# Optimization experiments

Hardware: AMD Instinct MI355X
Metric: run time of the kernel (lower is better)

The kernel has to match this reference:

```python
import jax, jax.numpy as jnp
import numpy as np

IN_DIM = 768
OUT_DIM = 768


def setup_inputs() -> dict:
    key = jax.random.key(0)
    k_x, k_q, k_k, k_v = jax.random.split(key, 4)
    B, S = 4, 4096
    x = jax.random.normal(k_x, (B, S, IN_DIM), dtype=jnp.float32)
    scale = 1.0 / np.sqrt(IN_DIM)
    Wq = jax.random.normal(k_q, (IN_DIM, OUT_DIM), dtype=jnp.float32) * scale
    Wk = jax.random.normal(k_k, (IN_DIM, OUT_DIM), dtype=jnp.float32) * scale
    Wv = jax.random.normal(k_v, (IN_DIM, OUT_DIM), dtype=jnp.float32) * scale
    return {"x": x, "Wq": Wq, "Wk": Wk, "Wv": Wv}


def reference(x, Wq, Wk, Wv):
    # x: [B, S, D_in]; W*: [D_in, D_out] (Linear without bias)
    q = jnp.einsum('bsd,de->bse', x, Wq)
    k = jnp.einsum('bsd,de->bse', x, Wk)
    v = jnp.einsum('bsd,de->bse', x, Wv)
    S = x.shape[1]
    scores = jnp.einsum('bqe,bke->bqk', q, k)  # [B, S, S]
    causal = jnp.tril(jnp.ones((S, S), dtype=bool))  # True where allowed
    scores = jnp.where(causal[None], scores, -jnp.inf)
    scale = 1.0 / jnp.sqrt(jnp.asarray(q.shape[-1], dtype=scores.dtype))
    weights = jax.nn.softmax(scores * scale, axis=-1)
    # dropout p=0.0 -> identity
    return jnp.einsum('bqk,bke->bqe', weights, v)
```

## Files before the change

kernel.cpp:

```cpp
#include <hip/hip_runtime.h>
#include <hip/hip_bf16.h>
#include <hip/hip_fp16.h>

#define DIM 768
#define SLEN 4096
#define BATCH 4
#define NTILES 528
#define NT256 136
#define SPB ((size_t)NTILES * 16384)

typedef __attribute__((ext_vector_type(8))) short short8;
typedef __attribute__((ext_vector_type(4))) short short4v;
typedef __attribute__((ext_vector_type(4))) float f32x4;
typedef __attribute__((ext_vector_type(8))) _Float16 f16x8;

typedef __attribute__((address_space(1))) void gvoid;
typedef __attribute__((address_space(3))) void lvoid;

__device__ __forceinline__ void gl_lds16(const void* g, void* l) {
  __builtin_amdgcn_global_load_lds((gvoid*)g, (lvoid*)l, 16, 0, 0);
}

__device__ __forceinline__ unsigned short f2h(float x) {
  union { _Float16 h; unsigned short u; } c; c.h = (_Float16)x; return c.u;
}
__device__ __forceinline__ float h2f(unsigned short u) {
  union { _Float16 h; unsigned short u; } c; c.u = u; return (float)c.h;
}

union V8 { short8 v; unsigned short u[8]; };

__global__ __launch_bounds__(256) void convert_x_kernel(
    const float* __restrict__ x, unsigned short* __restrict__ xb) {
  size_t i = ((size_t)blockIdx.x * 256 + threadIdx.x) * 8;
  f32x4 a = *(const f32x4*)(x + i);
  f32x4 b = *(const f32x4*)(x + i + 4);
  V8 o;
#pragma unroll
  for (int j = 0; j < 4; ++j) { o.u[j] = f2h(a[j]); o.u[4 + j] = f2h(b[j]); }
  *(short8*)(xb + i) = o.v;
}

__global__ __launch_bounds__(256) void transpose_w_kernel(
    const float* __restrict__ Wq, const float* __restrict__ Wk,
    const float* __restrict__ Wv, unsigned short* __restrict__ Wt) {
  __shared__ float Tl[32][33];
  const float* Wi = blockIdx.z == 0 ? Wq : (blockIdx.z == 1 ? Wk : Wv);
  unsigned short* Wo = Wt + (size_t)blockIdx.z * DIM * DIM;
  int k0 = blockIdx.x * 32, n0 = blockIdx.y * 32;
  int t = threadIdx.x;
  int r = t >> 3, c4 = (t & 7) * 4;
  f32x4 v = *(const f32x4*)(Wi + (size_t)(k0 + r) * DIM + n0 + c4);
#pragma unroll
  for (int j = 0; j < 4; ++j) Tl[r][c4 + j] = v[j];
  __syncthreads();
  short4v ov;
#pragma unroll
  for (int j = 0; j < 4; ++j) ov[j] = (short)f2h(Tl[c4 + j][r]);
  *(short4v*)(Wo + (size_t)(n0 + r) * DIM + k0 + c4) = ov;
}


#define STAGE(src, row0, kb, ldsoff)                                              \
  {                                                                               \
    gl_lds16((src) + (size_t)((row0) + rA) * DIM + (kb) + cA,                     \
             ldsb + (ldsoff) + t * 16);                                           \
    gl_lds16((src) + (size_t)((row0) + 64 + rA) * DIM + (kb) + cA,                \
             ldsb + (ldsoff) + 8192 + t * 16);                                    \
  }

#define STAGEP(srcp, stride, ldsoff)                                              \
  {                                                                               \
    gl_lds16((srcp) + (size_t)rA * (stride) + cA, ldsb + (ldsoff) + t * 16);      \
    gl_lds16((srcp) + (size_t)(64 + rA) * (stride) + cA,                          \
             ldsb + (ldsoff) + 8192 + t * 16);                                    \
  }

#define QPHASE(MH, CHB, STG, VMW)                                                 \
  {                                                                               \
    f16x8 afr[4];                                                                 \
    _Pragma("unroll") for (int j = 0; j < 4; ++j)                                 \
        afr[j] = __builtin_bit_cast(f16x8, *(const short8*)(ldsb + aB +           \
                 (MH) * 16384 + (j * 32 + arow) * 128 + (CHB)));                  \
    if ((MH) == 0) {                                                              \
      _Pragma("unroll") for (int n = 0; n < 4; ++n)                               \
          bfr[n] = __builtin_bit_cast(f16x8, *(const short8*)(ldsb + bB +         \
                   bh * 16384 + (brow + n * 16) * 128 + (CHB)));                  \
    }                                                                             \
    STG;                                                                          \
    VMW;                                                                          \
    asm volatile("s_barrier" ::: "memory");                                       \
    asm volatile("s_waitcnt lgkmcnt(0)" ::: "memory");                            \
    __builtin_amdgcn_sched_barrier(0);                                            \
    __builtin_amdgcn_s_setprio(1);                                                \
    _Pragma("unroll") for (int j = 0; j < 4; ++j)                                 \
      _Pragma("unroll") for (int n = 0; n < 4; ++n)                               \
        acc[(MH) * 4 + j][n] = __builtin_amdgcn_mfma_f32_16x16x32_f16(            \
            afr[j], bfr[n], acc[(MH) * 4 + j][n], 0, 0, 0);                       \
    __builtin_amdgcn_s_setprio(0);                                                \
    __builtin_amdgcn_sched_barrier(0);                                            \
    asm volatile("s_barrier" ::: "memory");                                       \
  }

template <int MODE>
__global__ __launch_bounds__(512, 2) void gemm8_kernel(
    const unsigned short* __restrict__ Ag, const unsigned short* __restrict__ Bg,
    unsigned short* __restrict__ o0, unsigned short* __restrict__ o1,
    unsigned short* __restrict__ o2, size_t stAB, size_t stS) {
  __shared__ __align__(16) unsigned short lds[65536];
  char* ldsb = (char*)lds;
  const int t = threadIdx.x;
  const int lane = t & 63, w = t >> 6;
  const int l15 = lane & 15, lg = lane >> 4;
  const int wr = w >> 2, wc = w & 3;

  int m0, n0, qt = 0, kt = 0, z = 0;
  const unsigned short *A, *B;
  unsigned short* Co = nullptr;
  unsigned short* Sb = nullptr;
  if (MODE == 0) {
    const int o = blockIdx.x;
    const int oi = (o & 7) * 72 + (o >> 3);
    const int mt = oi / 9, sub = oi - mt * 9;
    const int ntile = sub / 3;
    z = sub - ntile * 3;
    if (z < 2) {
      m0 = mt * 256; n0 = ntile * 256;
      A = Ag; B = Bg + (size_t)z * DIM * DIM;
      Co = z == 0 ? o0 : o1;
    } else {
      m0 = ntile * 256; n0 = mt * 256;
      A = Bg + (size_t)2 * DIM * DIM; B = Ag;
      Co = o2;
    }
  } else {
    const int i0 = blockIdx.x, b = blockIdx.y;
    const int i = (i0 & 7) * 17 + (i0 >> 3);
    qt = (int)((sqrtf(8.f * i + 1.f) - 1.f) * 0.5f);
    while ((qt + 1) * (qt + 2) / 2 <= i) ++qt;
    while (qt * (qt + 1) / 2 > i) --qt;
    kt = i - qt * (qt + 1) / 2;
    m0 = qt * 256; n0 = kt * 256;
    A = Ag + (size_t)b * stAB; B = Bg + (size_t)b * stAB;
    Sb = o0 + (size_t)b * stS;
  }

  const int rA = t >> 3;
  const int cA = (((t & 7) ^ ((t >> 3) & 7)) << 3);
  const int ch0 = ((lg ^ (l15 & 7)) << 4);
  const int arow = wr * 16 + l15;
  const int bh = wc >> 1;
  const int brow = (wc & 1) * 64 + l15;

  f32x4 acc[8][4];
#pragma unroll
  for (int f = 0; f < 8; ++f)
#pragma unroll
    for (int n = 0; n < 4; ++n) acc[f][n] = f32x4{0.f, 0.f, 0.f, 0.f};

  STAGE(A, m0, 0, 0);
  STAGE(B, n0, 0, 65536);
  STAGE(B, n0 + 128, 0, 65536 + 16384);
  STAGE(A, m0 + 128, 0, 16384);
  STAGE(B, n0, 64, 65536 + 32768);
  STAGE(A, m0, 64, 32768);
  asm volatile("s_waitcnt vmcnt(4)" ::: "memory");
  asm volatile("s_barrier" ::: "memory");

  for (int tt = 0; tt < 12; ++tt) {
    const int bt = tt & 1;
    const int aB = bt * 32768;
    const int bB = 65536 + bt * 32768;
    const int aN = (1 - bt) * 32768;
    const int bN = 65536 + (1 - bt) * 32768;
    const int kb1 = (tt + 1 < 12 ? tt + 1 : 11) * 64;
    const int kb2 = (tt + 2 < 12 ? tt + 2 : 11) * 64;
    f16x8 bfr[4];
    QPHASE(0, ch0,
           STAGE(B, n0 + 128, kb1, bN + 16384); STAGE(A, m0 + 128, kb1, aN + 16384),
           (void)0);
    QPHASE(1, ch0, (void)0, (void)0);
    QPHASE(0, ch0 ^ 64, (void)0, (void)0);
    QPHASE(1, ch0 ^ 64,
           STAGE(B, n0, kb2, bB); STAGE(A, m0, kb2, aB),
           asm volatile("s_waitcnt vmcnt(4)" ::: "memory"));
  }
  asm volatile("s_waitcnt vmcnt(0)" ::: "memory");

  if (MODE == 0) {
    if (z < 2) {
#pragma unroll
      for (int f = 0; f < 8; ++f) {
        const int row = m0 + f * 32 + wr * 16 + lg * 4;
#pragma unroll
        for (int n = 0; n < 4; ++n) {
          const int col = n0 + wc * 64 + n * 16 + l15;
#pragma unroll
          for (int ii = 0; ii < 4; ++ii)
            Co[(size_t)(row + ii) * DIM + col] = f2h(acc[f][n][ii]);
        }
      }
    } else {
      const int bb = n0 >> 12;
      unsigned short* O = Co + (size_t)bb * DIM * SLEN;
#pragma unroll
      for (int f = 0; f < 8; ++f) {
        const int row = m0 + f * 32 + wr * 16 + lg * 4;
#pragma unroll
        for (int n = 0; n < 4; ++n) {
          const int sl = (n0 + wc * 64 + n * 16 + l15) & (SLEN - 1);
#pragma unroll
          for (int ii = 0; ii < 4; ++ii)
            O[(size_t)(row + ii) * SLEN + sl] = f2h(acc[f][n][ii]);
        }
      }
    }
  } else {
#pragma unroll
    for (int f = 0; f < 8; ++f) {
      const int rl = (f * 32 + wr * 16 + lg * 4) & 127;
      const int Q128 = qt * 2 + (f >= 4 ? 1 : 0);
      const int K128 = kt * 2 + (wc >> 1);
      if (K128 > Q128) continue;
      const size_t tb = (size_t)(Q128 * (Q128 + 1) / 2 + K128) * 16384;
#pragma unroll
      for (int n = 0; n < 4; ++n) {
        const int cl = ((wc & 1) * 64 + n * 16 + l15);
#pragma unroll
        for (int ii = 0; ii < 4; ++ii)
          Sb[tb + (size_t)(rl + ii) * 128 + cl] = f2h(acc[f][n][ii]);
      }
    }
  }
}

__global__ __launch_bounds__(256) void softmax_kernel(
    unsigned short* __restrict__ S, size_t s_bstride) {
  __shared__ float redm[4], reds[4];
  const int r = blockIdx.x, b = blockIdx.y;
  unsigned short* Sb = S + (size_t)b * s_bstride;
  const int qt = r >> 7, rl = r & 127;
  const int ncols = (qt + 1) * 128;
  const size_t rowbase = (size_t)(qt * (qt + 1) / 2) * 16384 + (size_t)rl * 128;
  const int t = threadIdx.x, lane = t & 63, w = t >> 6;
  const int c0 = t * 16;
  const bool act = c0 < ncols;
  const float NEG = -3.0e38f;
  float sv[16];
  unsigned short* p = nullptr;
  if (act) {
    int ktile = c0 >> 7, cl = c0 & 127;
    p = Sb + rowbase + (size_t)ktile * 16384 + cl;
    V8 v0, v1; v0.v = *(const short8*)p; v1.v = *(const short8*)(p + 8);
#pragma unroll
    for (int j = 0; j < 8; ++j) {
      sv[j] = (c0 + j > r) ? NEG : h2f(v0.u[j]);
      sv[8 + j] = (c0 + 8 + j > r) ? NEG : h2f(v1.u[j]);
    }
  } else {
#pragma unroll
    for (int j = 0; j < 16; ++j) sv[j] = NEG;
  }
  float mx = NEG;
#pragma unroll
  for (int j = 0; j < 16; ++j) mx = fmaxf(mx, sv[j]);
#pragma unroll
  for (int d = 1; d < 64; d <<= 1) mx = fmaxf(mx, __shfl_xor(mx, d));
  if (lane == 0) redm[w] = mx;
  __syncthreads();
  mx = fmaxf(fmaxf(redm[0], redm[1]), fmaxf(redm[2], redm[3]));
  const float scl = 1.4426950408889634f / 27.712812921102035f;
  float e[16], sm = 0.f;
#pragma unroll
  for (int j = 0; j < 16; ++j) { e[j] = exp2f((sv[j] - mx) * scl); sm += e[j]; }
#pragma unroll
  for (int d = 1; d < 64; d <<= 1) sm += __shfl_xor(sm, d);
  if (lane == 0) reds[w] = sm;
  __syncthreads();
  float inv = 1.0f / (reds[0] + reds[1] + reds[2] + reds[3]);
  if (act) {
    V8 o0, o1;
#pragma unroll
    for (int j = 0; j < 8; ++j) { o0.u[j] = f2h(e[j] * inv); o1.u[j] = f2h(e[8 + j] * inv); }
    *(short8*)p = o0.v;
    *(short8*)(p + 8) = o1.v;
  }
}

__global__ __launch_bounds__(256) void zero_tile_kernel(unsigned short* __restrict__ z) {
  ((short8*)z)[blockIdx.x * 256 + threadIdx.x] = short8{0, 0, 0, 0, 0, 0, 0, 0};
}

__device__ const int pv_mt[24]  = {15,15,7,14,14,13,13,6,12,12,11,11,5,10,10,9,9,4,8,8,3,2,1,0};
__device__ const int pv_ks0[24] = {0,32,0,0,30,0,28,0,0,26,0,24,0,0,22,0,20,0,0,18,0,0,0,0};
__device__ const int pv_kl[24]  = {32,32,32,30,30,28,28,28,26,26,24,24,24,22,22,20,20,20,18,18,16,12,8,4};
__device__ const int pv_sec[24] = {0,1,0,0,1,0,1,0,0,1,0,1,0,0,1,0,1,0,0,1,0,0,0,0};

__global__ __launch_bounds__(512, 2) void pv256_kernel(
    const unsigned short* __restrict__ S, const unsigned short* __restrict__ Vt,
    const unsigned short* __restrict__ Zt, float* __restrict__ Out,
    float* __restrict__ Part) {
  __shared__ __align__(16) unsigned short lds[65536];
  char* ldsb = (char*)lds;
  const int t = threadIdx.x, lane = t & 63, w = t >> 6;
  const int l15 = lane & 15, lg = lane >> 4;
  const int wr = w >> 2, wc = w & 3;
  const int rank = blockIdx.x / 12, sub = blockIdx.x % 12;
  const int b = sub / 3, nt = sub % 3;
  const int mt = pv_mt[rank], ks0 = pv_ks0[rank], kl = pv_kl[rank];
  const int sec = pv_sec[rank];
  const int q0 = 2 * mt, q1 = 2 * mt + 1;
  const int kend = ks0 + kl;
  const unsigned short* Sbb = S + (size_t)b * SPB;
  const unsigned short* Vb = Vt + (size_t)b * DIM * SLEN + (size_t)(nt * 256) * SLEN;

  auto asrc = [&](int ks, int qh) -> const unsigned short* {
    const int K128 = ks >> 1;
    const unsigned short* base =
        (K128 <= qh) ? Sbb + (size_t)(qh * (qh + 1) / 2 + K128) * 16384 : Zt;
    return base + (ks & 1) * 64;
  };

  const int rA = t >> 3;
  const int cA = (((t & 7) ^ ((t >> 3) & 7)) << 3);
  const int ch0 = ((lg ^ (l15 & 7)) << 4);
  const int arow = wr * 16 + l15;
  const int bh = wc >> 1;
  const int brow = (wc & 1) * 64 + l15;

  f32x4 acc[8][4];
#pragma unroll
  for (int f = 0; f < 8; ++f)
#pragma unroll
    for (int n = 0; n < 4; ++n) acc[f][n] = f32x4{0.f, 0.f, 0.f, 0.f};

  const int ksp = (ks0 + 1 < kend) ? ks0 + 1 : kend - 1;
  STAGEP(asrc(ks0, q0), 128, 0);
  STAGEP(Vb + (size_t)ks0 * 64, SLEN, 65536);
  STAGEP(Vb + (size_t)128 * SLEN + (size_t)ks0 * 64, SLEN, 65536 + 16384);
  STAGEP(asrc(ks0, q1), 128, 16384);
  STAGEP(Vb + (size_t)ksp * 64, SLEN, 65536 + 32768);
  STAGEP(asrc(ksp, q0), 128, 32768);
  asm volatile("s_waitcnt vmcnt(4)" ::: "memory");
  asm volatile("s_barrier" ::: "memory");

  for (int it = 0; it < kl; ++it) {
    const int ts = ks0 + it;
    const int bt = it & 1;
    const int aB = bt * 32768;
    const int bB = 65536 + bt * 32768;
    const int aN = (1 - bt) * 32768;
    const int bN = 65536 + (1 - bt) * 32768;
    const int t1 = (ts + 1 < kend) ? ts + 1 : kend - 1;
    const int t2 = (ts + 2 < kend) ? ts + 2 : kend - 1;
    f16x8 bfr[4];
    QPHASE(0, ch0,
           STAGEP(Vb + (size_t)128 * SLEN + (size_t)t1 * 64, SLEN, bN + 16384);
           STAGEP(asrc(t1, q1), 128, aN + 16384),
           (void)0);
    QPHASE(1, ch0, (void)0, (void)0);
    QPHASE(0, ch0 ^ 64, (void)0, (void)0);
    QPHASE(1, ch0 ^ 64,
           STAGEP(Vb + (size_t)t2 * 64, SLEN, bB);
           STAGEP(asrc(t2, q0), 128, aB),
           asm volatile("s_waitcnt vmcnt(4)" ::: "memory"));
  }
  asm volatile("s_waitcnt vmcnt(0)" ::: "memory");

  if (!sec) {
    float* Ob = Out + (size_t)b * SLEN * DIM + (size_t)(mt * 256) * DIM + nt * 256;
#pragma unroll
    for (int f = 0; f < 8; ++f) {
      const int rl = f * 32 + wr * 16 + lg * 4;
#pragma unroll
      for (int n = 0; n < 4; ++n) {
        const int cl = wc * 64 + n * 16 + l15;
#pragma unroll
        for (int ii = 0; ii < 4; ++ii)
          Ob[(size_t)(rl + ii) * DIM + cl] = acc[f][n][ii];
      }
    }
  } else {
    float* Pb = Part + (size_t)((b * 3 + nt) * 8 + (mt - 8)) * 65536;
#pragma unroll
    for (int f = 0; f < 8; ++f) {
      const int rl = f * 32 + wr * 16 + lg * 4;
#pragma unroll
      for (int n = 0; n < 4; ++n) {
        const int cl = wc * 64 + n * 16 + l15;
#pragma unroll
        for (int ii = 0; ii < 4; ++ii)
          Pb[(size_t)(rl + ii) * 256 + cl] = acc[f][n][ii];
      }
    }
  }
}

__global__ __launch_bounds__(256) void pv_reduce_kernel(
    const float* __restrict__ Part, float* __restrict__ Out) {
  const int bx = blockIdx.x;
  const int p = bx >> 6;
  const int within = ((bx & 63) * 256 + threadIdx.x) * 4;
  const int mt = 8 + (p & 7);
  const int bnt = p >> 3, b = bnt / 3, nt = bnt % 3;
  const int r = within >> 8, c = within & 255;
  float* o = Out + (size_t)b * SLEN * DIM + (size_t)(mt * 256 + r) * DIM + nt * 256 + c;
  const f32x4 pv = *(const f32x4*)(Part + (size_t)p * 65536 + within);
  const f32x4 ov = *(const f32x4*)o;
  *(f32x4*)o = ov + pv;
}

__global__ __launch_bounds__(256) void gemm_pv_kernel(
    const unsigned short* __restrict__ S, const unsigned short* __restrict__ Vt,
    float* __restrict__ Out, size_t s_bstride, int nb) {
  __shared__ __align__(16) unsigned short As[4096], Bs[4096];
  const int idx = blockIdx.x;
  const int qtr = idx / (6 * nb);
  const int rem = idx - qtr * 6 * nb;
  const int b = rem / 6, nt = rem % 6;
  const int qt = 31 - qtr;
  const unsigned short* Sb = S + (size_t)b * s_bstride + (size_t)(qt * (qt + 1) / 2) * 16384;
  const unsigned short* Vb = Vt + (size_t)b * DIM * SLEN + (size_t)(nt * 128) * SLEN;
  float* Ob = Out + (size_t)b * SLEN * DIM + (size_t)(qt * 128) * DIM + nt * 128;
  const int t = threadIdx.x, lane = t & 63, w = t >> 6;
  const int l15 = lane & 15, lg = lane >> 4;
  const int wm = w >> 1, wn = w & 1;
  f32x4 acc[4][4];
#pragma unroll
  for (int a = 0; a < 4; ++a)
#pragma unroll
    for (int b2 = 0; b2 < 4; ++b2) acc[a][b2] = f32x4{0.f, 0.f, 0.f, 0.f};
  const int c0 = t, c1 = t + 256;
  const int r0 = c0 >> 2, k80 = (c0 & 3) * 8;
  const int r1 = c1 >> 2, k81 = (c1 & 3) * 8;
  const int ksteps = (qt + 1) * 4;
  for (int ks = 0; ks < ksteps; ++ks) {
    const int kb = ks * 32;
    const size_t atile = (size_t)(kb >> 7) * 16384 + (size_t)(kb & 127);
    __syncthreads();
    gl_lds16(Sb + atile + (size_t)r0 * 128 + k80, As + (size_t)c0 * 8);
    gl_lds16(Sb + atile + (size_t)r1 * 128 + k81, As + (size_t)c1 * 8);
    gl_lds16(Vb + (size_t)r0 * SLEN + kb + k80, Bs + (size_t)c0 * 8);
    gl_lds16(Vb + (size_t)r1 * SLEN + kb + k81, Bs + (size_t)c1 * 8);
    __syncthreads();
    f16x8 a[4], bf[4];
#pragma unroll
    for (int mi = 0; mi < 4; ++mi)
      a[mi] = __builtin_bit_cast(f16x8, *(const short8*)(As + (wm * 64 + mi * 16 + l15) * 32 + lg * 8));
#pragma unroll
    for (int ni = 0; ni < 4; ++ni)
      bf[ni] = __builtin_bit_cast(f16x8, *(const short8*)(Bs + (wn * 64 + ni * 16 + l15) * 32 + lg * 8));
#pragma unroll
    for (int mi = 0; mi < 4; ++mi)
#pragma unroll
      for (int ni = 0; ni < 4; ++ni)
        acc[mi][ni] = __builtin_amdgcn_mfma_f32_16x16x32_f16(a[mi], bf[ni], acc[mi][ni], 0, 0, 0);
  }
#pragma unroll
  for (int mi = 0; mi < 4; ++mi)
#pragma unroll
    for (int ni = 0; ni < 4; ++ni)
#pragma unroll
      for (int ii = 0; ii < 4; ++ii) {
        int rl = wm * 64 + mi * 16 + lg * 4 + ii;
        int cl = wn * 64 + ni * 16 + l15;
        Ob[(size_t)rl * DIM + cl] = acc[mi][ni][ii];
      }
}

extern "C" void kernel_launch(void* const* d_in, const int* in_sizes, int n_in,
                              void* d_out, int out_size, void* d_ws, size_t ws_size,
                              hipStream_t stream) {
  const float* x  = (const float*)d_in[0];
  const float* Wq = (const float*)d_in[1];
  const float* Wk = (const float*)d_in[2];
  const float* Wv = (const float*)d_in[3];
  float* out = (float*)d_out;

  const size_t n_x = (size_t)BATCH * SLEN * DIM;
  unsigned short* Q  = (unsigned short*)d_ws;
  unsigned short* K  = Q + n_x;
  unsigned short* Vt = K + n_x;
  unsigned short* xb = Vt + n_x;
  unsigned short* wt = xb + n_x;
  const size_t base_elems = 4 * n_x + (size_t)3 * DIM * DIM;
  const bool full = ws_size >= (base_elems + 4 * SPB) * 2;

  convert_x_kernel<<<dim3((unsigned)(n_x / 8 / 256)), 256, 0, stream>>>(x, xb);
  transpose_w_kernel<<<dim3(DIM / 32, DIM / 32, 3), 256, 0, stream>>>(Wq, Wk, Wv, wt);

  gemm8_kernel<0><<<dim3(576), 512, 0, stream>>>(xb, wt, Q, K, Vt, 0, 0);

  if (full) {
    unsigned short* S = (unsigned short*)d_ws + base_elems;
    zero_tile_kernel<<<8, 256, 0, stream>>>(wt);
    gemm8_kernel<1><<<dim3(NT256, BATCH), 512, 0, stream>>>(
        Q, K, S, nullptr, nullptr, (size_t)SLEN * DIM, SPB);
    softmax_kernel<<<dim3(SLEN, BATCH), 256, 0, stream>>>(S, SPB);
    pv256_kernel<<<dim3(288), 512, 0, stream>>>(S, Vt, wt, out, (float*)xb);
    pv_reduce_kernel<<<dim3(6144), 256, 0, stream>>>((const float*)xb, out);
  } else {
    unsigned short* S = xb;
    for (int b = 0; b < BATCH; ++b) {
      const size_t qo = (size_t)b * SLEN * DIM;
      gemm8_kernel<1><<<dim3(NT256, 1), 512, 0, stream>>>(
          Q + qo, K + qo, S, nullptr, nullptr, 0, 0);
      softmax_kernel<<<dim3(SLEN, 1), 256, 0, stream>>>(S, 0);
      gemm_pv_kernel<<<dim3(32 * 6), 256, 0, stream>>>(
          S, Vt + (size_t)b * DIM * SLEN, out + qo, 0, 1);
    }
  }
}
```

Measured before the change: 294.4 us.

## Restructure GEMM K-loop into single-barrier tile body with interleaved LDS reads

```diff
diff --git a/kernel.cpp b/kernel.cpp
--- a/kernel.cpp
+++ b/kernel.cpp
@@ -76,29 +76,44 @@
              ldsb + (ldsoff) + 8192 + t * 16);                                    \
   }
 
-#define QPHASE(MH, CHB, STG, VMW)                                                 \
+#define RDA(dst, base, chb)                                                       \
+  _Pragma("unroll") for (int j = 0; j < 4; ++j)                                   \
+      dst[j] = __builtin_bit_cast(f16x8, *(const short8*)(ldsb + (base) +         \
+               (j * 32 + arow) * 128 + (chb)));
+
+#define RDB(dst, base, chb)                                                       \
+  _Pragma("unroll") for (int n = 0; n < 4; ++n)                                   \
+      dst[n] = __builtin_bit_cast(f16x8, *(const short8*)(ldsb + (base) +         \
+               bh * 16384 + (brow + n * 16) * 128 + (chb)));
+
+#define MFMA16(af, bf, FO)                                                        \
+  __builtin_amdgcn_s_setprio(1);                                                  \
+  _Pragma("unroll") for (int j = 0; j < 4; ++j)                                   \
+    _Pragma("unroll") for (int n = 0; n < 4; ++n)                                 \
+      acc[(FO) + j][n] = __builtin_amdgcn_mfma_f32_16x16x32_f16(                  \
+          af[j], bf[n], acc[(FO) + j][n], 0, 0, 0);                               \
+  __builtin_amdgcn_s_setprio(0);
+
+#define LGKM(N)                                                                   \
+  asm volatile("s_waitcnt lgkmcnt(" #N ")" ::: "memory");                         \
+  __builtin_amdgcn_sched_barrier(0);
+
+#define TILE_BODY(aBx, bBx, STGB, STGA)                                           \
   {                                                                               \
-    f16x8 afr[4];                                                                 \
-    _Pragma("unroll") for (int j = 0; j < 4; ++j)                                 \
-        afr[j] = __builtin_bit_cast(f16x8, *(const short8*)(ldsb + aB +           \
-                 (MH) * 16384 + (j * 32 + arow) * 128 + (CHB)));                  \
-    if ((MH) == 0) {                                                              \
-      _Pragma("unroll") for (int n = 0; n < 4; ++n)                               \
-          bfr[n] = __builtin_bit_cast(f16x8, *(const short8*)(ldsb + bB +         \
-                   bh * 16384 + (brow + n * 16) * 128 + (CHB)));                  \
-    }                                                                             \
-    STG;                                                                          \
-    VMW;                                                                          \
-    asm volatile("s_barrier" ::: "memory");                                       \
-    asm volatile("s_waitcnt lgkmcnt(0)" ::: "memory");                            \
-    __builtin_amdgcn_sched_barrier(0);                                            \
-    __builtin_amdgcn_s_setprio(1);                                                \
-    _Pragma("unroll") for (int j = 0; j < 4; ++j)                                 \
-      _Pragma("unroll") for (int n = 0; n < 4; ++n)                               \
-        acc[(MH) * 4 + j][n] = __builtin_amdgcn_mfma_f32_16x16x32_f16(            \
-            afr[j], bfr[n], acc[(MH) * 4 + j][n], 0, 0, 0);                       \
-    __builtin_amdgcn_s_setprio(0);                                                \
-    __builtin_amdgcn_sched_barrier(0);                                            \
+    f16x8 a0_[4], a1_[4], a2_[4], a3_[4], b0_[4], b2_[4];                         \
+    RDA(a0_, (aBx), ch0);                                                         \
+    RDB(b0_, (bBx), ch0);                                                         \
+    RDA(a1_, (aBx) + 16384, ch0);                                                 \
+    STGB;                                                                         \
+    LGKM(4); MFMA16(a0_, b0_, 0);                                                 \
+    RDA(a2_, (aBx), ch0 ^ 64);                                                    \
+    RDB(b2_, (bBx), ch0 ^ 64);                                                    \
+    STGA;                                                                         \
+    LGKM(8); MFMA16(a1_, b0_, 4);                                                 \
+    RDA(a3_, (aBx) + 16384, ch0 ^ 64);                                            \
+    LGKM(4); MFMA16(a2_, b2_, 0);                                                 \
+    LGKM(0); MFMA16(a3_, b2_, 4);                                                 \
+    asm volatile("s_waitcnt vmcnt(0)" ::: "memory");                              \
     asm volatile("s_barrier" ::: "memory");                                       \
   }
 
@@ -159,12 +174,10 @@
     for (int n = 0; n < 4; ++n) acc[f][n] = f32x4{0.f, 0.f, 0.f, 0.f};
 
   STAGE(A, m0, 0, 0);
+  STAGE(A, m0 + 128, 0, 16384);
   STAGE(B, n0, 0, 65536);
   STAGE(B, n0 + 128, 0, 65536 + 16384);
-  STAGE(A, m0 + 128, 0, 16384);
-  STAGE(B, n0, 64, 65536 + 32768);
-  STAGE(A, m0, 64, 32768);
-  asm volatile("s_waitcnt vmcnt(4)" ::: "memory");
+  asm volatile("s_waitcnt vmcnt(0)" ::: "memory");
   asm volatile("s_barrier" ::: "memory");
 
   for (int tt = 0; tt < 12; ++tt) {
@@ -174,18 +187,10 @@
     const int aN = (1 - bt) * 32768;
     const int bN = 65536 + (1 - bt) * 32768;
     const int kb1 = (tt + 1 < 12 ? tt + 1 : 11) * 64;
-    const int kb2 = (tt + 2 < 12 ? tt + 2 : 11) * 64;
-    f16x8 bfr[4];
-    QPHASE(0, ch0,
-           STAGE(B, n0 + 128, kb1, bN + 16384); STAGE(A, m0 + 128, kb1, aN + 16384),
-           (void)0);
-    QPHASE(1, ch0, (void)0, (void)0);
-    QPHASE(0, ch0 ^ 64, (void)0, (void)0);
-    QPHASE(1, ch0 ^ 64,
-           STAGE(B, n0, kb2, bB); STAGE(A, m0, kb2, aB),
-           asm volatile("s_waitcnt vmcnt(4)" ::: "memory"));
-  }
-  asm volatile("s_waitcnt vmcnt(0)" ::: "memory");
+    TILE_BODY(aB, bB,
+              STAGE(B, n0, kb1, bN); STAGE(B, n0 + 128, kb1, bN + 16384),
+              STAGE(A, m0, kb1, aN); STAGE(A, m0 + 128, kb1, aN + 16384));
+  }
 
   if (MODE == 0) {
     if (z < 2) {
@@ -334,14 +339,11 @@
 #pragma unroll
     for (int n = 0; n < 4; ++n) acc[f][n] = f32x4{0.f, 0.f, 0.f, 0.f};
 
-  const int ksp = (ks0 + 1 < kend) ? ks0 + 1 : kend - 1;
   STAGEP(asrc(ks0, q0), 128, 0);
+  STAGEP(asrc(ks0, q1), 128, 16384);
   STAGEP(Vb + (size_t)ks0 * 64, SLEN, 65536);
   STAGEP(Vb + (size_t)128 * SLEN + (size_t)ks0 * 64, SLEN, 65536 + 16384);
-  STAGEP(asrc(ks0, q1), 128, 16384);
-  STAGEP(Vb + (size_t)ksp * 64, SLEN, 65536 + 32768);
-  STAGEP(asrc(ksp, q0), 128, 32768);
-  asm volatile("s_waitcnt vmcnt(4)" ::: "memory");
+  asm volatile("s_waitcnt vmcnt(0)" ::: "memory");
   asm volatile("s_barrier" ::: "memory");
 
   for (int it = 0; it < kl; ++it) {
@@ -352,20 +354,12 @@
     const int aN = (1 - bt) * 32768;
     const int bN = 65536 + (1 - bt) * 32768;
     const int t1 = (ts + 1 < kend) ? ts + 1 : kend - 1;
-    const int t2 = (ts + 2 < kend) ? ts + 2 : kend - 1;
-    f16x8 bfr[4];
-    QPHASE(0, ch0,
-           STAGEP(Vb + (size_t)128 * SLEN + (size_t)t1 * 64, SLEN, bN + 16384);
-           STAGEP(asrc(t1, q1), 128, aN + 16384),
-           (void)0);
-    QPHASE(1, ch0, (void)0, (void)0);
-    QPHASE(0, ch0 ^ 64, (void)0, (void)0);
-    QPHASE(1, ch0 ^ 64,
-           STAGEP(Vb + (size_t)t2 * 64, SLEN, bB);
-           STAGEP(asrc(t2, q0), 128, aB),
-           asm volatile("s_waitcnt vmcnt(4)" ::: "memory"));
-  }
-  asm volatile("s_waitcnt vmcnt(0)" ::: "memory");
+    TILE_BODY(aB, bB,
+              STAGEP(Vb + (size_t)t1 * 64, SLEN, bN);
+              STAGEP(Vb + (size_t)128 * SLEN + (size_t)t1 * 64, SLEN, bN + 16384),
+              STAGEP(asrc(t1, q0), 128, aN);
+              STAGEP(asrc(t1, q1), 128, aN + 16384));
+  }
 
   if (!sec) {
     float* Ob = Out + (size_t)b * SLEN * DIM + (size_t)(mt * 256) * DIM + nt * 256;
```

New measurement: 278.3 us, median of 3. 1.06x faster.
